# Kernel tuning notes

Hardware: AMD Instinct MI355X
Metric: run time of the kernel (lower is better)

Reference implementation:

```python
import jax, jax.numpy as jnp
import numpy as np

N = 8192      # batch (subjects)
XD = 32       # covariate dim
LD = 32       # encoder latent dim
HD = 128      # odefunc hidden dim
TD = 3        # trans_dim (illness-death model)
NH = 3        # number_of_hazards (allowed transitions)
NP = TD * TD  # num_probs
G = 256       # time grid intervals -> 257 unique times incl. 0
DT = 0.01
STATE = 2 * NP + NH  # [P | P^-1 | cum hazards] = 21


def setup_inputs() -> dict:
    rng = np.random.default_rng(0)
    x = rng.standard_normal((N, XD)).astype(np.float32)
    times = (np.arange(G + 1) * DT).astype(np.float32)  # unique grid incl. t=0
    si = rng.integers(0, G, size=N)
    ei = si + 1 + (rng.random(N) * (G - si)).astype(np.int64)  # ei in (si, G]
    tstart = times[si]
    tstop = times[ei]
    fs = rng.integers(1, 3, size=N)  # from_state in {1,2}
    ts = np.where(fs == 1, rng.integers(2, 4, size=N), 3)  # valid transitions
    # allowed transitions of [[0,1,1],[0,0,1],[0,0,0]]
    trans_rows = np.array([0, 0, 1], dtype=np.int32)
    trans_cols = np.array([1, 2, 2], dtype=np.int32)

    def lin(k, fi, fo, s=1.0):
        r = np.random.default_rng(k)
        return (r.standard_normal((fi, fo)).astype(np.float32) * s / np.sqrt(fi),
                np.zeros(fo, dtype=np.float32))
    enc_W1, enc_b1 = lin(1, XD, 64)
    enc_W2, enc_b2 = lin(2, 64, LD)
    net_W1, net_b1 = lin(3, STATE + LD + XD + 1, HD)
    net_W2, net_b2 = lin(4, HD, 2 * NH, s=0.5)
    return {
        "x": jnp.asarray(x), "tstart": jnp.asarray(tstart), "tstop": jnp.asarray(tstop),
        "from_state": jnp.asarray(fs, jnp.int64), "to_state": jnp.asarray(ts, jnp.int64),
        "tstart_idx": jnp.asarray(si, jnp.int64), "tstop_idx": jnp.asarray(ei, jnp.int64),
        "times": jnp.asarray(times), "trans_rows": jnp.asarray(trans_rows),
        "trans_cols": jnp.asarray(trans_cols),
        "enc_W1": jnp.asarray(enc_W1), "enc_b1": jnp.asarray(enc_b1),
        "enc_W2": jnp.asarray(enc_W2), "enc_b2": jnp.asarray(enc_b2),
        "net_W1": jnp.asarray(net_W1), "net_b1": jnp.asarray(net_b1),
        "net_W2": jnp.asarray(net_W2), "net_b2": jnp.asarray(net_b2),
    }


def reference(x, tstart, tstop, from_state, to_state, tstart_idx, tstop_idx, times,
              trans_rows, trans_cols, enc_W1, enc_b1, enc_W2, enc_b2,
              net_W1, net_b1, net_W2, net_b2):
    n = x.shape[0]
    z = jnp.tanh(x @ enc_W1 + enc_b1) @ enc_W2 + enc_b2  # encoder(x): [n, LD]

    def net(h):  # odefunc.net
        return jnp.tanh(h @ net_W1 + net_b1) @ net_W2 + net_b2

    di = jnp.arange(TD)

    def qmat(qvec, with_diag):
        # scatter hazards into [n,3,3] transition-rate matrix (mask positions)
        Q = jnp.zeros((n, TD, TD), qvec.dtype).at[:, trans_rows, trans_cols].set(qvec)
        if with_diag:
            Q = Q.at[:, di, di].set(-jnp.sum(Q, axis=-1))
        return Q

    # ODE state: [ vec(P(0,t)) | vec(P(0,t)^-1) | cumulative hazards ]
    P0 = jnp.tile(jnp.eye(TD, dtype=x.dtype).reshape(-1), (n, 1))
    state0 = jnp.concatenate([P0, P0, jnp.zeros((n, NH), x.dtype)], axis=1)

    def deriv(state, t):
        P = state[:, :NP].reshape(n, TD, TD)
        Tinv = state[:, NP:2 * NP].reshape(n, TD, TD)
        h = jnp.concatenate([state, z, x, jnp.full((n, 1), t, x.dtype)], axis=1)
        qvec = jax.nn.softplus(net(h)[:, :NH])  # softplus_beta = 1
        Q = qmat(qvec, True)
        dP = jnp.einsum('nij,njk->nik', P, Q)      # dP/dt = P Q
        dTinv = -jnp.einsum('nij,njk->nik', Q, Tinv)  # d(P^-1)/dt = -Q P^-1
        return jnp.concatenate([dP.reshape(n, -1), dTinv.reshape(n, -1), qvec], axis=1)

    def step(state, tdt):
        t, dt = tdt
        new = state + dt * deriv(state, t)  # explicit Euler on the event grid
        return new, new

    dts = times[1:] - times[:-1]
    _, outs = jax.lax.scan(step, state0, (times[:-1], dts))
    out = jnp.concatenate([state0[None], outs], axis=0)  # [T, n, STATE]

    ar = jnp.arange(n)
    # vectorized replacement of the per-sample python-loop gathers
    Tinv_start = out[tstart_idx, ar, NP:2 * NP].reshape(n, TD, TD)
    T_stop = out[tstop_idx, ar, :NP].reshape(n, TD, TD)
    Sfull = jnp.einsum('nij,njk->nik', Tinv_start, T_stop)
    fi = from_state - 1
    ti = to_state - 1
    S = Sfull[ar, fi, fi]

    state_stop = out[tstop_idx, ar, :]
    h1 = jnp.concatenate([state_stop, z, x, tstop[:, None]], axis=1)
    qvec = jax.nn.softplus(net(h1)[:, :NH])
    q = qmat(qvec, False)  # forward() does NOT fill the diagonal here
    lam = q[ar, fi, ti]

    h2 = jnp.concatenate([out[-1], z, x, jnp.full((n, 1), jnp.max(tstop), x.dtype)], axis=1)
    all_hazards_T = net(h2)[:, NH:]
    return S, lam, all_hazards_T
```

## Files before the change

### kernel.cpp

```cpp
#include <hip/hip_runtime.h>

#define NSAMP 8192
#define GSTEP 256

typedef __attribute__((ext_vector_type(8))) short short8;
typedef __attribute__((ext_vector_type(4))) float f32x4;

__device__ __forceinline__ float fast_tanh(float x) {
    float e = __expf(2.0f * x);
    return 1.0f - 2.0f * __builtin_amdgcn_rcpf(1.0f + e);
}
__device__ __forceinline__ float softplus_f(float x) {
    return __logf(1.0f + __expf(x));
}
__device__ __forceinline__ unsigned pk_bf16(float a, float b) {
    unsigned r;
    asm("v_cvt_pk_bf16_f32 %0, %1, %2" : "=v"(r) : "v"(a), "v"(b));
    return r;
}
union frag_u { unsigned u[4]; short8 s; };

__device__ __forceinline__ void split8(const float* v, short8& H, short8& L) {
    frag_u Hu, Lu;
    #pragma unroll
    for (int r = 0; r < 4; ++r) {
        float a = v[2 * r], b = v[2 * r + 1];
        unsigned h = pk_bf16(a, b);
        float ha = __int_as_float(h << 16);
        float hb = __int_as_float(h & 0xffff0000u);
        Hu.u[r] = h;
        Lu.u[r] = pk_bf16(a - ha, b - hb);
    }
    H = Hu.s; L = Lu.s;
}

__global__ void tmax_k(const float* __restrict__ tstop, float* __restrict__ ws) {
    __shared__ float sm[16];
    float m = -1e30f;
    for (int i = threadIdx.x; i < NSAMP; i += 1024) m = fmaxf(m, tstop[i]);
    #pragma unroll
    for (int o = 32; o > 0; o >>= 1) m = fmaxf(m, __shfl_down(m, o, 64));
    if ((threadIdx.x & 63) == 0) sm[threadIdx.x >> 6] = m;
    __syncthreads();
    if (threadIdx.x == 0) {
        float r = sm[0];
        for (int w = 1; w < 16; ++w) r = fmaxf(r, sm[w]);
        ws[0] = r;
    }
}

__global__ void enc_k(const float* __restrict__ x,
                      const float* __restrict__ eW1, const float* __restrict__ eb1,
                      const float* __restrict__ eW2, const float* __restrict__ eb2,
                      float* __restrict__ zout) {
    int s = blockIdx.x * 256 + threadIdx.x;
    float xv[32];
    #pragma unroll
    for (int i = 0; i < 8; ++i) {
        float4 v = reinterpret_cast<const float4*>(x)[s * 8 + i];
        xv[4*i+0] = v.x; xv[4*i+1] = v.y; xv[4*i+2] = v.z; xv[4*i+3] = v.w;
    }
    float z[32];
    #pragma unroll
    for (int o = 0; o < 32; ++o) z[o] = eb2[o];
    #pragma unroll 4
    for (int h = 0; h < 64; ++h) {
        float a = eb1[h];
        #pragma unroll
        for (int i = 0; i < 32; ++i) a += xv[i] * eW1[i * 64 + h];
        float th = fast_tanh(a);
        #pragma unroll
        for (int o = 0; o < 32; ++o) z[o] += th * eW2[h * 32 + o];
    }
    #pragma unroll
    for (int o = 0; o < 32; ++o) zout[s * 32 + o] = z[o];
}

__global__ void __launch_bounds__(256, 2)
surv_k(const float* __restrict__ x,
       const float* __restrict__ tstop,
       const int* __restrict__ fsv, const int* __restrict__ tsv,
       const int* __restrict__ siv, const int* __restrict__ eiv,
       const float* __restrict__ W1, const float* __restrict__ b1,
       const float* __restrict__ W2, const float* __restrict__ b2,
       const float* __restrict__ wsf,
       float* __restrict__ out)
{
    __shared__ __align__(16) float qred[2][6][16][4];
    const int tid = threadIdx.x;
    const int w   = tid >> 6;
    const int l   = tid & 63;
    const int a   = l >> 4;
    const int col = l & 15;
    const int s   = blockIdx.x * 16 + col;

    short8 Ah[2], Al[2];
    #pragma unroll
    for (int tt = 0; tt < 2; ++tt) {
        const int j = (2 * w + tt) * 16 + col;
        float av[8];
        #pragma unroll
        for (int i = 0; i < 8; ++i) {
            int k = a * 8 + i;
            float v = 0.f;
            if (k < 21) v = W1[k * 128 + j];
            else if (k == 21) v = W1[85 * 128 + j];
            av[i] = v;
        }
        split8(av, Ah[tt], Al[tt]);
    }

    float W2r[2][4][3];
    #pragma unroll
    for (int tt = 0; tt < 2; ++tt)
        #pragma unroll
        for (int r = 0; r < 4; ++r) {
            int jd = (2 * w + tt) * 16 + a * 4 + r;
            #pragma unroll
            for (int c = 0; c < 3; ++c) W2r[tt][r][c] = W2[jd * 6 + c];
        }
    const float b2r0 = b2[0], b2r1 = b2[1], b2r2 = b2[2];

    float cfr[2][4];
    #pragma unroll
    for (int tt = 0; tt < 2; ++tt)
        #pragma unroll
        for (int r = 0; r < 4; ++r)
            cfr[tt][r] = b1[(2 * w + tt) * 16 + a * 4 + r];
    {
        const float* z  = wsf + 16 + s * 32;
        const float* xs = x + s * 32;
        for (int i = 0; i < 32; ++i) {
            float zi = z[i];
            float xi = xs[i];
            #pragma unroll
            for (int tt = 0; tt < 2; ++tt)
                #pragma unroll
                for (int r = 0; r < 4; ++r) {
                    int jd = (2 * w + tt) * 16 + a * 4 + r;
                    cfr[tt][r] = fmaf(zi, W1[(21 + i) * 128 + jd],
                                 fmaf(xi, W1[(53 + i) * 128 + jd], cfr[tt][r]));
                }
        }
    }

    const int si = siv[s], ei = eiv[s];

    float st[22];
    #pragma unroll
    for (int k = 0; k < 22; ++k) st[k] = 0.f;
    st[0] = st[4] = st[8] = 1.f;
    st[9] = st[13] = st[17] = 1.f;
    float Tsnap[9], Ssnap[21];
    #pragma unroll
    for (int k = 0; k < 9; ++k) Tsnap[k] = 0.f;
    #pragma unroll
    for (int k = 0; k < 21; ++k) Ssnap[k] = 0.f;

    int buf = 0;
    for (int m = 0; m < GSTEP; ++m) {
        if (__any((m == si) || (m == ei))) {
            if (m == si) {
                #pragma unroll
                for (int k = 0; k < 9; ++k) Tsnap[k] = st[9 + k];
            }
            if (m == ei) {
                #pragma unroll
                for (int k = 0; k < 21; ++k) Ssnap[k] = st[k];
            }
        }
        st[21] = (float)m * 0.01f;

        float sv[8];
        #pragma unroll
        for (int i = 0; i < 8; ++i) {
            float x01 = (a == 0) ? st[i] : st[8 + i];
            float x2  = (i < 6) ? st[16 + i] : 0.f;
            sv[i] = (a < 2) ? x01 : ((a == 2) ? x2 : 0.f);
        }
        short8 Bh, Bl;
        split8(sv, Bh, Bl);

        float p0 = 0.f, p1 = 0.f, p2 = 0.f;
        #pragma unroll
        for (int tt = 0; tt < 2; ++tt) {
            f32x4 acc = {cfr[tt][0], cfr[tt][1], cfr[tt][2], cfr[tt][3]};
            acc = __builtin_amdgcn_mfma_f32_16x16x32_bf16(Ah[tt], Bh, acc, 0, 0, 0);
            acc = __builtin_amdgcn_mfma_f32_16x16x32_bf16(Ah[tt], Bl, acc, 0, 0, 0);
            acc = __builtin_amdgcn_mfma_f32_16x16x32_bf16(Al[tt], Bh, acc, 0, 0, 0);
            #pragma unroll
            for (int r = 0; r < 4; ++r) {
                float t_ = fast_tanh(acc[r]);
                p0 = fmaf(t_, W2r[tt][r][0], p0);
                p1 = fmaf(t_, W2r[tt][r][1], p1);
                p2 = fmaf(t_, W2r[tt][r][2], p2);
            }
        }
        p0 += __shfl_xor(p0, 16, 64); p0 += __shfl_xor(p0, 32, 64);
        p1 += __shfl_xor(p1, 16, 64); p1 += __shfl_xor(p1, 32, 64);
        p2 += __shfl_xor(p2, 16, 64); p2 += __shfl_xor(p2, 32, 64);
        if (l < 16) {
            qred[buf][0][col][w] = p0;
            qred[buf][1][col][w] = p1;
            qred[buf][2][col][w] = p2;
        }
        __syncthreads();
        float4 v0 = *reinterpret_cast<const float4*>(&qred[buf][0][col][0]);
        float4 v1 = *reinterpret_cast<const float4*>(&qred[buf][1][col][0]);
        float4 v2 = *reinterpret_cast<const float4*>(&qred[buf][2][col][0]);
        buf ^= 1;
        float q0d = 0.01f * softplus_f(v0.x + v0.y + v0.z + v0.w + b2r0);
        float q1d = 0.01f * softplus_f(v1.x + v1.y + v1.z + v1.w + b2r1);
        float q2d = 0.01f * softplus_f(v2.x + v2.y + v2.z + v2.w + b2r2);
        float qsd = q0d + q1d;

        #pragma unroll
        for (int i = 0; i < 3; ++i) {
            float Pi0 = st[3*i], Pi1 = st[3*i+1];
            st[3*i+0] = fmaf(-qsd, Pi0, st[3*i+0]);
            st[3*i+1] = fmaf(-q2d, Pi1, fmaf(q0d, Pi0, st[3*i+1]));
            st[3*i+2] = fmaf( q2d, Pi1, fmaf(q1d, Pi0, st[3*i+2]));
        }
        #pragma unroll
        for (int k = 0; k < 3; ++k) {
            float T0 = st[9+k], T1 = st[12+k], T2 = st[15+k];
            st[9+k]  = fmaf(-q1d, T2, fmaf(-q0d, T1, fmaf(qsd, T0, st[9+k])));
            st[12+k] = fmaf(q2d, T1 - T2, st[12+k]);
        }
        st[18] += q0d; st[19] += q1d; st[20] += q2d;
    }
    if (ei == GSTEP) {
        #pragma unroll
        for (int k = 0; k < 21; ++k) Ssnap[k] = st[k];
    }

    float W2e[2][4][6];
    #pragma unroll
    for (int tt = 0; tt < 2; ++tt)
        #pragma unroll
        for (int r = 0; r < 4; ++r) {
            int jd = (2 * w + tt) * 16 + a * 4 + r;
            #pragma unroll
            for (int c = 0; c < 6; ++c) W2e[tt][r][c] = W2[jd * 6 + c];
        }
    float b2e[6];
    #pragma unroll
    for (int c = 0; c < 6; ++c) b2e[c] = b2[c];

    auto net6 = [&](const float* hs, int bb, float* o6) {
        float sv[8];
        #pragma unroll
        for (int i = 0; i < 8; ++i) {
            float x01 = (a == 0) ? hs[i] : hs[8 + i];
            float x2  = (i < 6) ? hs[16 + i] : 0.f;
            sv[i] = (a < 2) ? x01 : ((a == 2) ? x2 : 0.f);
        }
        short8 Bh, Bl;
        split8(sv, Bh, Bl);
        float pk6[6] = {0.f, 0.f, 0.f, 0.f, 0.f, 0.f};
        #pragma unroll
        for (int tt = 0; tt < 2; ++tt) {
            f32x4 acc = {cfr[tt][0], cfr[tt][1], cfr[tt][2], cfr[tt][3]};
            acc = __builtin_amdgcn_mfma_f32_16x16x32_bf16(Ah[tt], Bh, acc, 0, 0, 0);
            acc = __builtin_amdgcn_mfma_f32_16x16x32_bf16(Ah[tt], Bl, acc, 0, 0, 0);
            acc = __builtin_amdgcn_mfma_f32_16x16x32_bf16(Al[tt], Bh, acc, 0, 0, 0);
            #pragma unroll
            for (int r = 0; r < 4; ++r) {
                float t_ = fast_tanh(acc[r]);
                #pragma unroll
                for (int c = 0; c < 6; ++c) pk6[c] = fmaf(t_, W2e[tt][r][c], pk6[c]);
            }
        }
        #pragma unroll
        for (int c = 0; c < 6; ++c) {
            pk6[c] += __shfl_xor(pk6[c], 16, 64);
            pk6[c] += __shfl_xor(pk6[c], 32, 64);
        }
        if (l < 16) {
            #pragma unroll
            for (int c = 0; c < 6; ++c) qred[bb][c][col][w] = pk6[c];
        }
        __syncthreads();
        #pragma unroll
        for (int c = 0; c < 6; ++c) {
            float4 v = *reinterpret_cast<const float4*>(&qred[bb][c][col][0]);
            o6[c] = v.x + v.y + v.z + v.w + b2e[c];
        }
    };

    float h1[22], h2[22];
    #pragma unroll
    for (int k = 0; k < 21; ++k) h1[k] = Ssnap[k];
    h1[21] = tstop[s];
    #pragma unroll
    for (int k = 0; k < 21; ++k) h2[k] = st[k];
    h2[21] = wsf[0];

    float l2a[6], l2b[6];
    net6(h1, 0, l2a);
    net6(h2, 1, l2b);

    int fi = fsv[s] - 1;
    int ti = tsv[s] - 1;
    float Sv = 0.f;
    #pragma unroll
    for (int j = 0; j < 3; ++j)
        Sv = fmaf(Tsnap[fi * 3 + j], Ssnap[3 * j + fi], Sv);

    float qv0 = softplus_f(l2a[0]), qv1 = softplus_f(l2a[1]), qv2 = softplus_f(l2a[2]);
    float lam = (fi == 0) ? ((ti == 1) ? qv0 : ((ti == 2) ? qv1 : 0.0f))
                          : ((fi == 1 && ti == 2) ? qv2 : 0.0f);

    if (w == 0 && l < 16) {
        out[s]                     = Sv;
        out[NSAMP + s]             = lam;
        out[2 * NSAMP + 3 * s + 0] = l2b[3];
        out[2 * NSAMP + 3 * s + 1] = l2b[4];
        out[2 * NSAMP + 3 * s + 2] = l2b[5];
    }
}

extern "C" void kernel_launch(void* const* d_in, const int* in_sizes, int n_in,
                              void* d_out, int out_size, void* d_ws, size_t ws_size,
                              hipStream_t stream) {
    const float* x     = (const float*)d_in[0];
    const float* tstop = (const float*)d_in[2];
    const int*   fs    = (const int*)d_in[3];
    const int*   ts    = (const int*)d_in[4];
    const int*   si    = (const int*)d_in[5];
    const int*   ei    = (const int*)d_in[6];
    const float* eW1   = (const float*)d_in[10];
    const float* eb1   = (const float*)d_in[11];
    const float* eW2   = (const float*)d_in[12];
    const float* eb2   = (const float*)d_in[13];
    const float* W1    = (const float*)d_in[14];
    const float* b1    = (const float*)d_in[15];
    const float* W2    = (const float*)d_in[16];
    const float* b2    = (const float*)d_in[17];
    float* wsf = (float*)d_ws;
    float* out = (float*)d_out;

    tmax_k<<<1, 1024, 0, stream>>>(tstop, wsf);
    enc_k<<<32, 256, 0, stream>>>(x, eW1, eb1, eW2, eb2, wsf + 16);
    surv_k<<<512, 256, 0, stream>>>(x, tstop, fs, ts, si, ei,
                                    W1, b1, W2, b2, wsf, out);
}
```

Before: 453.2 us.

## Run whole ODE MLP per 16-sample tile in one wavefront with MFMA second layer

The survival kernel moves from four wavefronts per 16-sample block to a single 64-lane wavefront that holds all eight hidden-dimension tiles of W1. This removes the per-step LDS reduction and __syncthreads barrier. The second layer (hidden to 6 hazards) now runs as bf16 MFMAs instead of scalar FMAs plus shuffle reductions. The constant z/x contribution is precomputed with MFMAs, and tanh/softplus are rewritten with folded log2(e) scaling on the raw v_exp/v_log instructions. In exchange there are fewer waves per block (512 single-wave blocks), more register pressure, and a longer serial MFMA chain per step, so there is less latency hiding, plus some lost precision from the bf16 second layer.

```diff
diff --git a/kernel.cpp b/kernel.cpp
--- a/kernel.cpp
+++ b/kernel.cpp
@@ -2,29 +2,34 @@
 
 #define NSAMP 8192
 #define GSTEP 256
+#define SCL   2.8853900817779268f
+#define L2E   1.4426950408889634f
+#define LN2   0.69314718055994531f
+#define LN2DT 0.0069314718055994531f
 
 typedef __attribute__((ext_vector_type(8))) short short8;
 typedef __attribute__((ext_vector_type(4))) float f32x4;
 
+__device__ __forceinline__ float exp2_hw(float x){ float r; asm("v_exp_f32 %0, %1" : "=v"(r) : "v"(x)); return r; }
+__device__ __forceinline__ float log2_hw(float x){ float r; asm("v_log_f32 %0, %1" : "=v"(r) : "v"(x)); return r; }
+__device__ __forceinline__ unsigned pk_bf16(float a, float b){ unsigned r; asm("v_cvt_pk_bf16_f32 %0, %1, %2" : "=v"(r) : "v"(a), "v"(b)); return r; }
+
+__device__ __forceinline__ float tanh_scl(float y) {
+    float e = exp2_hw(y);
+    return fmaf(-2.0f, __builtin_amdgcn_rcpf(1.0f + e), 1.0f);
+}
 __device__ __forceinline__ float fast_tanh(float x) {
-    float e = __expf(2.0f * x);
-    return 1.0f - 2.0f * __builtin_amdgcn_rcpf(1.0f + e);
-}
-__device__ __forceinline__ float softplus_f(float x) {
-    return __logf(1.0f + __expf(x));
-}
-__device__ __forceinline__ unsigned pk_bf16(float a, float b) {
-    unsigned r;
-    asm("v_cvt_pk_bf16_f32 %0, %1, %2" : "=v"(r) : "v"(a), "v"(b));
-    return r;
-}
+    float e = exp2_hw(x * SCL);
+    return fmaf(-2.0f, __builtin_amdgcn_rcpf(1.0f + e), 1.0f);
+}
+
 union frag_u { unsigned u[4]; short8 s; };
 
 __device__ __forceinline__ void split8(const float* v, short8& H, short8& L) {
     frag_u Hu, Lu;
     #pragma unroll
     for (int r = 0; r < 4; ++r) {
-        float a = v[2 * r], b = v[2 * r + 1];
+        float a = v[2*r], b = v[2*r+1];
         unsigned h = pk_bf16(a, b);
         float ha = __int_as_float(h << 16);
         float hb = __int_as_float(h & 0xffff0000u);
@@ -76,7 +81,7 @@
     for (int o = 0; o < 32; ++o) zout[s * 32 + o] = z[o];
 }
 
-__global__ void __launch_bounds__(256, 2)
+__global__ void __launch_bounds__(64, 1)
 surv_k(const float* __restrict__ x,
        const float* __restrict__ tstop,
        const int* __restrict__ fsv, const int* __restrict__ tsv,
@@ -86,63 +91,118 @@
        const float* __restrict__ wsf,
        float* __restrict__ out)
 {
-    __shared__ __align__(16) float qred[2][6][16][4];
-    const int tid = threadIdx.x;
-    const int w   = tid >> 6;
-    const int l   = tid & 63;
+    const int l   = threadIdx.x;
     const int a   = l >> 4;
     const int col = l & 15;
     const int s   = blockIdx.x * 16 + col;
 
-    short8 Ah[2], Al[2];
-    #pragma unroll
-    for (int tt = 0; tt < 2; ++tt) {
-        const int j = (2 * w + tt) * 16 + col;
+    short8 A1h[8], A1l[8];
+    #pragma unroll
+    for (int tt = 0; tt < 8; ++tt) {
         float av[8];
         #pragma unroll
         for (int i = 0; i < 8; ++i) {
             int k = a * 8 + i;
             float v = 0.f;
-            if (k < 21) v = W1[k * 128 + j];
-            else if (k == 21) v = W1[85 * 128 + j];
-            av[i] = v;
-        }
-        split8(av, Ah[tt], Al[tt]);
-    }
-
-    float W2r[2][4][3];
-    #pragma unroll
-    for (int tt = 0; tt < 2; ++tt)
-        #pragma unroll
-        for (int r = 0; r < 4; ++r) {
-            int jd = (2 * w + tt) * 16 + a * 4 + r;
-            #pragma unroll
-            for (int c = 0; c < 3; ++c) W2r[tt][r][c] = W2[jd * 6 + c];
-        }
-    const float b2r0 = b2[0], b2r1 = b2[1], b2r2 = b2[2];
-
-    float cfr[2][4];
-    #pragma unroll
-    for (int tt = 0; tt < 2; ++tt)
-        #pragma unroll
-        for (int r = 0; r < 4; ++r)
-            cfr[tt][r] = b1[(2 * w + tt) * 16 + a * 4 + r];
+            if (k < 21) v = W1[k * 128 + tt * 16 + col];
+            else if (k == 21) v = W1[85 * 128 + tt * 16 + col];
+            av[i] = v * SCL;
+        }
+        split8(av, A1h[tt], A1l[tt]);
+    }
+
+    short8 A2f[4];
     {
-        const float* z  = wsf + 16 + s * 32;
-        const float* xs = x + s * 32;
-        for (int i = 0; i < 32; ++i) {
-            float zi = z[i];
-            float xi = xs[i];
-            #pragma unroll
-            for (int tt = 0; tt < 2; ++tt)
+        int  cc  = (col < 6) ? col : 0;
+        bool cok = (col < 6);
+        float csc = (col < 3) ? L2E : 1.0f;
+        #pragma unroll
+        for (int j = 0; j < 4; ++j) {
+            frag_u F;
+            #pragma unroll
+            for (int rr = 0; rr < 4; ++rr) {
+                int e0 = 2 * rr, e1 = e0 + 1;
+                int h0 = j * 32 + (e0 >> 2) * 16 + a * 4 + (e0 & 3);
+                int h1 = j * 32 + (e1 >> 2) * 16 + a * 4 + (e1 & 3);
+                float w0 = cok ? W2[h0 * 6 + cc] * csc : 0.f;
+                float w1 = cok ? W2[h1 * 6 + cc] * csc : 0.f;
+                F.u[rr] = pk_bf16(w0, w1);
+            }
+            A2f[j] = F.s;
+        }
+    }
+    float c2i[4];
+    #pragma unroll
+    for (int r = 0; r < 4; ++r) {
+        int row = a * 4 + r;
+        float bv = (row < 6) ? b2[row] : 0.f;
+        c2i[r] = (row < 3) ? bv * L2E : bv;
+    }
+
+    f32x4 cf[8];
+    #pragma unroll
+    for (int tt = 0; tt < 8; ++tt) {
+        cf[tt] = f32x4{ b1[tt*16 + a*4 + 0], b1[tt*16 + a*4 + 1],
+                        b1[tt*16 + a*4 + 2], b1[tt*16 + a*4 + 3] };
+    }
+    {
+        const float* zp = wsf + 16 + s * 32;
+        const float* xp = x + s * 32;
+        #pragma unroll
+        for (int j = 0; j < 2; ++j) {
+            float bv[8];
+            #pragma unroll
+            for (int i = 0; i < 8; ++i) bv[i] = (j == 0) ? zp[a*8 + i] : xp[a*8 + i];
+            short8 Bh, Bl; split8(bv, Bh, Bl);
+            #pragma unroll
+            for (int tt = 0; tt < 8; ++tt) {
+                float av[8];
                 #pragma unroll
-                for (int r = 0; r < 4; ++r) {
-                    int jd = (2 * w + tt) * 16 + a * 4 + r;
-                    cfr[tt][r] = fmaf(zi, W1[(21 + i) * 128 + jd],
-                                 fmaf(xi, W1[(53 + i) * 128 + jd], cfr[tt][r]));
-                }
-        }
-    }
+                for (int i = 0; i < 8; ++i)
+                    av[i] = W1[(21 + j*32 + a*8 + i) * 128 + tt * 16 + col];
+                short8 Ah, Al; split8(av, Ah, Al);
+                cf[tt] = __builtin_amdgcn_mfma_f32_16x16x32_bf16(Ah, Bh, cf[tt], 0,0,0);
+                cf[tt] = __builtin_amdgcn_mfma_f32_16x16x32_bf16(Ah, Bl, cf[tt], 0,0,0);
+                cf[tt] = __builtin_amdgcn_mfma_f32_16x16x32_bf16(Al, Bh, cf[tt], 0,0,0);
+            }
+        }
+        #pragma unroll
+        for (int tt = 0; tt < 8; ++tt)
+            #pragma unroll
+            for (int r = 0; r < 4; ++r) cf[tt][r] *= SCL;
+    }
+
+    auto run_net = [&](const float* hs) -> f32x4 {
+        float sv[8];
+        #pragma unroll
+        for (int i = 0; i < 8; ++i) {
+            float x01 = (a == 0) ? hs[i] : hs[8 + i];
+            float x2  = (i < 6) ? hs[16 + i] : 0.f;
+            sv[i] = (a < 2) ? x01 : ((a == 2) ? x2 : 0.f);
+        }
+        short8 Bh, Bl; split8(sv, Bh, Bl);
+        f32x4 acc[8];
+        #pragma unroll
+        for (int tt = 0; tt < 8; ++tt) {
+            acc[tt] = cf[tt];
+            acc[tt] = __builtin_amdgcn_mfma_f32_16x16x32_bf16(A1h[tt], Bh, acc[tt], 0,0,0);
+            acc[tt] = __builtin_amdgcn_mfma_f32_16x16x32_bf16(A1h[tt], Bl, acc[tt], 0,0,0);
+            acc[tt] = __builtin_amdgcn_mfma_f32_16x16x32_bf16(A1l[tt], Bh, acc[tt], 0,0,0);
+        }
+        f32x4 a2 = { c2i[0], c2i[1], c2i[2], c2i[3] };
+        #pragma unroll
+        for (int j = 0; j < 4; ++j) {
+            frag_u F;
+            #pragma unroll
+            for (int rr = 0; rr < 4; ++rr) {
+                int tile = 2 * j + (rr >> 1);
+                int r0 = 2 * (rr & 1);
+                F.u[rr] = pk_bf16(tanh_scl(acc[tile][r0]), tanh_scl(acc[tile][r0 + 1]));
+            }
+            a2 = __builtin_amdgcn_mfma_f32_16x16x32_bf16(A2f[j], F.s, a2, 0,0,0);
+        }
+        return a2;
+    };
 
     const int si = siv[s], ei = eiv[s];
 
@@ -157,7 +217,6 @@
     #pragma unroll
     for (int k = 0; k < 21; ++k) Ssnap[k] = 0.f;
 
-    int buf = 0;
     for (int m = 0; m < GSTEP; ++m) {
         if (__any((m == si) || (m == ei))) {
             if (m == si) {
@@ -171,47 +230,13 @@
         }
         st[21] = (float)m * 0.01f;
 
-        float sv[8];
-        #pragma unroll
-        for (int i = 0; i < 8; ++i) {
-            float x01 = (a == 0) ? st[i] : st[8 + i];
-            float x2  = (i < 6) ? st[16 + i] : 0.f;
-            sv[i] = (a < 2) ? x01 : ((a == 2) ? x2 : 0.f);
-        }
-        short8 Bh, Bl;
-        split8(sv, Bh, Bl);
-
-        float p0 = 0.f, p1 = 0.f, p2 = 0.f;
-        #pragma unroll
-        for (int tt = 0; tt < 2; ++tt) {
-            f32x4 acc = {cfr[tt][0], cfr[tt][1], cfr[tt][2], cfr[tt][3]};
-            acc = __builtin_amdgcn_mfma_f32_16x16x32_bf16(Ah[tt], Bh, acc, 0, 0, 0);
-            acc = __builtin_amdgcn_mfma_f32_16x16x32_bf16(Ah[tt], Bl, acc, 0, 0, 0);
-            acc = __builtin_amdgcn_mfma_f32_16x16x32_bf16(Al[tt], Bh, acc, 0, 0, 0);
-            #pragma unroll
-            for (int r = 0; r < 4; ++r) {
-                float t_ = fast_tanh(acc[r]);
-                p0 = fmaf(t_, W2r[tt][r][0], p0);
-                p1 = fmaf(t_, W2r[tt][r][1], p1);
-                p2 = fmaf(t_, W2r[tt][r][2], p2);
-            }
-        }
-        p0 += __shfl_xor(p0, 16, 64); p0 += __shfl_xor(p0, 32, 64);
-        p1 += __shfl_xor(p1, 16, 64); p1 += __shfl_xor(p1, 32, 64);
-        p2 += __shfl_xor(p2, 16, 64); p2 += __shfl_xor(p2, 32, 64);
-        if (l < 16) {
-            qred[buf][0][col][w] = p0;
-            qred[buf][1][col][w] = p1;
-            qred[buf][2][col][w] = p2;
-        }
-        __syncthreads();
-        float4 v0 = *reinterpret_cast<const float4*>(&qred[buf][0][col][0]);
-        float4 v1 = *reinterpret_cast<const float4*>(&qred[buf][1][col][0]);
-        float4 v2 = *reinterpret_cast<const float4*>(&qred[buf][2][col][0]);
-        buf ^= 1;
-        float q0d = 0.01f * softplus_f(v0.x + v0.y + v0.z + v0.w + b2r0);
-        float q1d = 0.01f * softplus_f(v1.x + v1.y + v1.z + v1.w + b2r1);
-        float q2d = 0.01f * softplus_f(v2.x + v2.y + v2.z + v2.w + b2r2);
+        f32x4 a2 = run_net(st);
+        float y0 = __shfl(a2[0], col, 64);
+        float y1 = __shfl(a2[1], col, 64);
+        float y2 = __shfl(a2[2], col, 64);
+        float q0d = LN2DT * log2_hw(1.0f + exp2_hw(y0));
+        float q1d = LN2DT * log2_hw(1.0f + exp2_hw(y1));
+        float q2d = LN2DT * log2_hw(1.0f + exp2_hw(y2));
         float qsd = q0d + q1d;
 
         #pragma unroll
@@ -234,71 +259,26 @@
         for (int k = 0; k < 21; ++k) Ssnap[k] = st[k];
     }
 
-    float W2e[2][4][6];
-    #pragma unroll
-    for (int tt = 0; tt < 2; ++tt)
-        #pragma unroll
-        for (int r = 0; r < 4; ++r) {
-            int jd = (2 * w + tt) * 16 + a * 4 + r;
-            #pragma unroll
-            for (int c = 0; c < 6; ++c) W2e[tt][r][c] = W2[jd * 6 + c];
-        }
-    float b2e[6];
-    #pragma unroll
-    for (int c = 0; c < 6; ++c) b2e[c] = b2[c];
-
-    auto net6 = [&](const float* hs, int bb, float* o6) {
-        float sv[8];
-        #pragma unroll
-        for (int i = 0; i < 8; ++i) {
-            float x01 = (a == 0) ? hs[i] : hs[8 + i];
-            float x2  = (i < 6) ? hs[16 + i] : 0.f;
-            sv[i] = (a < 2) ? x01 : ((a == 2) ? x2 : 0.f);
-        }
-        short8 Bh, Bl;
-        split8(sv, Bh, Bl);
-        float pk6[6] = {0.f, 0.f, 0.f, 0.f, 0.f, 0.f};
-        #pragma unroll
-        for (int tt = 0; tt < 2; ++tt) {
-            f32x4 acc = {cfr[tt][0], cfr[tt][1], cfr[tt][2], cfr[tt][3]};
-            acc = __builtin_amdgcn_mfma_f32_16x16x32_bf16(Ah[tt], Bh, acc, 0, 0, 0);
-            acc = __builtin_amdgcn_mfma_f32_16x16x32_bf16(Ah[tt], Bl, acc, 0, 0, 0);
-            acc = __builtin_amdgcn_mfma_f32_16x16x32_bf16(Al[tt], Bh, acc, 0, 0, 0);
-            #pragma unroll
-            for (int r = 0; r < 4; ++r) {
-                float t_ = fast_tanh(acc[r]);
-                #pragma unroll
-                for (int c = 0; c < 6; ++c) pk6[c] = fmaf(t_, W2e[tt][r][c], pk6[c]);
-            }
-        }
-        #pragma unroll
-        for (int c = 0; c < 6; ++c) {
-            pk6[c] += __shfl_xor(pk6[c], 16, 64);
-            pk6[c] += __shfl_xor(pk6[c], 32, 64);
-        }
-        if (l < 16) {
-            #pragma unroll
-            for (int c = 0; c < 6; ++c) qred[bb][c][col][w] = pk6[c];
-        }
-        __syncthreads();
-        #pragma unroll
-        for (int c = 0; c < 6; ++c) {
-            float4 v = *reinterpret_cast<const float4*>(&qred[bb][c][col][0]);
-            o6[c] = v.x + v.y + v.z + v.w + b2e[c];
-        }
-    };
-
-    float h1[22], h2[22];
+    float h1[22];
     #pragma unroll
     for (int k = 0; k < 21; ++k) h1[k] = Ssnap[k];
     h1[21] = tstop[s];
+    f32x4 e1 = run_net(h1);
+    float ya = __shfl(e1[0], col, 64);
+    float yb = __shfl(e1[1], col, 64);
+    float yc = __shfl(e1[2], col, 64);
+    float qv0 = LN2 * log2_hw(1.0f + exp2_hw(ya));
+    float qv1 = LN2 * log2_hw(1.0f + exp2_hw(yb));
+    float qv2 = LN2 * log2_hw(1.0f + exp2_hw(yc));
+
+    float h2[22];
     #pragma unroll
     for (int k = 0; k < 21; ++k) h2[k] = st[k];
     h2[21] = wsf[0];
-
-    float l2a[6], l2b[6];
-    net6(h1, 0, l2a);
-    net6(h2, 1, l2b);
+    f32x4 e2 = run_net(h2);
+    float hz3 = __shfl(e2[3], col, 64);
+    float hz4 = __shfl(e2[0], 16 + col, 64);
+    float hz5 = __shfl(e2[1], 16 + col, 64);
 
     int fi = fsv[s] - 1;
     int ti = tsv[s] - 1;
@@ -306,17 +286,15 @@
     #pragma unroll
     for (int j = 0; j < 3; ++j)
         Sv = fmaf(Tsnap[fi * 3 + j], Ssnap[3 * j + fi], Sv);
-
-    float qv0 = softplus_f(l2a[0]), qv1 = softplus_f(l2a[1]), qv2 = softplus_f(l2a[2]);
     float lam = (fi == 0) ? ((ti == 1) ? qv0 : ((ti == 2) ? qv1 : 0.0f))
                           : ((fi == 1 && ti == 2) ? qv2 : 0.0f);
 
-    if (w == 0 && l < 16) {
+    if (l < 16) {
         out[s]                     = Sv;
         out[NSAMP + s]             = lam;
-        out[2 * NSAMP + 3 * s + 0] = l2b[3];
-        out[2 * NSAMP + 3 * s + 1] = l2b[4];
-        out[2 * NSAMP + 3 * s + 2] = l2b[5];
+        out[2 * NSAMP + 3 * s + 0] = hz3;
+        out[2 * NSAMP + 3 * s + 1] = hz4;
+        out[2 * NSAMP + 3 * s + 2] = hz5;
     }
 }
 
@@ -342,6 +320,6 @@
 
     tmax_k<<<1, 1024, 0, stream>>>(tstop, wsf);
     enc_k<<<32, 256, 0, stream>>>(x, eW1, eb1, eW2, eb2, wsf + 16);
-    surv_k<<<512, 256, 0, stream>>>(x, tstop, fs, ts, si, ei,
-                                    W1, b1, W2, b2, wsf, out);
-}
+    surv_k<<<512, 64, 0, stream>>>(x, tstop, fs, ts, si, ei,
+                                   W1, b1, W2, b2, wsf, out);
+}
```

After: 381.1 us. 1.19x faster.
